# Optimization experiments

Measured on AMD Instinct MI355X. Metric: run time of the kernel, lower is better.

The kernel has to match this reference:

```python
import jax, jax.numpy as jnp
import numpy as np

TAU = 2.0
THR = 0.5
ALPHA = 4.0  # Sigmoid_Grad surrogate sharpness
EPS = 1e-5
HEADS = 16
SCALE = 0.25

@jax.custom_vjp
def spike(v):
    return (v > 0.0).astype(v.dtype)

def _spike_fwd(v):
    return (v > 0.0).astype(v.dtype), v

def _spike_bwd(v, g):
    s = jax.nn.sigmoid(ALPHA * v)
    return (g * ALPHA * s * (1.0 - s),)

spike.defvjp(_spike_fwd, _spike_bwd)

def lif(x):
    # x: (T, ...) ; stateful LIF over leading time dim, hard reset (detached spike)
    def step(mem, xt):
        mem = mem + (xt - mem) / TAU
        s = spike(mem - THR)
        mem = mem * (1.0 - jax.lax.stop_gradient(s))
        return mem, s
    _, s = jax.lax.scan(step, jnp.zeros_like(x[0]), x)
    return s

def bn(x, p):
    # x: (T,B,C,N), p: (4,C) = (gamma, beta, mean, var); inference-form BatchNorm1d
    g, b, m, v = p
    shp = (1, 1, -1, 1)
    return (x - m.reshape(shp)) * (g.reshape(shp) / jnp.sqrt(v.reshape(shp) + EPS)) + b.reshape(shp)

def conv_bn_lif(x, w, p, bias=None):
    # 1x1 Conv1d == channel matmul: (T,B,Cin,N) x (Cout,Cin) -> (T,B,Cout,N)
    y = jnp.einsum('tbcn,oc->tbon', x, w)
    if bias is not None:
        y = y + bias.reshape(1, 1, -1, 1)
    return lif(bn(y, p))

def _block(x, q_w, q_bn, k_w, k_bn, v_w, v_bn, proj_w, proj_bn,
           fc1_w, fc1_b, fc1_bn, fc2_w, fc2_b, fc2_bn):
    T, B, C, N = x.shape
    D = C // HEADS

    def to_heads(y):  # (T,B,C,N) -> (T,B,H,N,D)
        return y.transpose(0, 1, 3, 2).reshape(T, B, N, HEADS, D).transpose(0, 1, 3, 2, 4)

    q = to_heads(conv_bn_lif(x, q_w, q_bn))
    k = to_heads(conv_bn_lif(x, k_w, k_bn))
    v = to_heads(conv_bn_lif(x, v_w, v_bn))

    attn = jnp.einsum('tbhnd,tbhmd->tbhnm', q, k) * SCALE  # no softmax
    r = jnp.einsum('tbhnm,tbhmd->tbhnd', attn, v) * SCALE
    r = r.transpose(0, 1, 2, 4, 3).reshape(T, B, C, N)  # (T,B,H,D,N) -> (T,B,C,N)
    r = lif(r)  # attn_lif
    attn_out = conv_bn_lif(r, proj_w, proj_bn)  # proj conv+bn+lif

    x = x + attn_out  # residual 1

    h = conv_bn_lif(x, fc1_w, fc1_bn, fc1_b)
    m = conv_bn_lif(h, fc2_w, fc2_bn, fc2_b)
    return x + m  # residual 2

def setup_inputs() -> dict:
    key = jax.random.key(0)
    ks = jax.random.split(key, 16)
    T, B, C, N = 4, 16, 256, 512
    H = 1024  # mlp hidden = 4*C
    w = 0.05
    d = {}
    d['x'] = jax.random.normal(ks[0], (T, B, C, N), jnp.float32)
    d['q_w'] = jax.random.normal(ks[1], (C, C), jnp.float32) * w
    d['q_bn'] = jax.random.uniform(ks[2], (4, C), jnp.float32, 0.5, 1.5)
    d['k_w'] = jax.random.normal(ks[3], (C, C), jnp.float32) * w
    d['k_bn'] = jax.random.uniform(ks[4], (4, C), jnp.float32, 0.5, 1.5)
    d['v_w'] = jax.random.normal(ks[5], (C, C), jnp.float32) * w
    d['v_bn'] = jax.random.uniform(ks[6], (4, C), jnp.float32, 0.5, 1.5)
    d['proj_w'] = jax.random.normal(ks[7], (C, C), jnp.float32) * w
    d['proj_bn'] = jax.random.uniform(ks[8], (4, C), jnp.float32, 0.5, 1.5)
    d['fc1_w'] = jax.random.normal(ks[9], (H, C), jnp.float32) * w
    d['fc1_b'] = jnp.zeros((H,), jnp.float32)
    d['fc1_bn'] = jax.random.uniform(ks[10], (4, H), jnp.float32, 0.5, 1.5)
    d['fc2_w'] = jax.random.normal(ks[11], (C, H), jnp.float32) * w
    d['fc2_b'] = jnp.zeros((C,), jnp.float32)
    d['fc2_bn'] = jax.random.uniform(ks[12], (4, C), jnp.float32, 0.5, 1.5)
    return d

def reference(x, q_w, q_bn, k_w, k_bn, v_w, v_bn, proj_w, proj_bn,
              fc1_w, fc1_b, fc1_bn, fc2_w, fc2_b, fc2_bn):
    return _block(x, q_w, q_bn, k_w, k_bn, v_w, v_bn, proj_w, proj_bn,
                  fc1_w, fc1_b, fc1_bn, fc2_w, fc2_b, fc2_bn)
```

## Files before the change

kernel.cpp:

```cpp
#include <hip/hip_runtime.h>

#pragma clang fp contract(off)

typedef unsigned char u8;
typedef unsigned int u32;

#define TSTEPS 4

template <int XMODE, bool HASX2, int OMODE>
__global__ __launch_bounds__(256) void conv_bn_lif(
    const void* __restrict__ X1v, const u8* __restrict__ X2,
    const float* __restrict__ Wt, const float* __restrict__ bias,
    const float* __restrict__ bnp,
    u8* __restrict__ Sout,
    const float* __restrict__ Xres, const u8* __restrict__ AOres,
    float* __restrict__ Fout,
    int Bsz, int Cin, int Cout, int N)
{
  const int tid = threadIdx.x;
  const int tx = tid & 15, ty = tid >> 4;
  const int nBase = blockIdx.x * 64, oBase = blockIdx.y * 64, b = blockIdx.z;
  const int KT = Cin >> 5;
  const int TT = TSTEPS * KT;

  __shared__ __align__(16) float Xs[2][32][68];
  __shared__ __align__(16) float Ws[2][32][68];

  float sc[4], mn[4], bt[4], bi[4];
  #pragma unroll
  for (int i = 0; i < 4; ++i) {
    int o = oBase + ty * 4 + i;
    float g  = bnp[0 * Cout + o];
    float be = bnp[1 * Cout + o];
    float m  = bnp[2 * Cout + o];
    float vv = bnp[3 * Cout + o];
    float d_f = (float)((double)vv + (double)1e-5f);
    float s_f = (float)sqrt((double)d_f);
    sc[i] = (float)((double)g / (double)s_f);
    mn[i] = m; bt[i] = be;
    bi[i] = bias ? bias[o] : 0.0f;
  }

  float mem[4][4], acc[4][4];
  #pragma unroll
  for (int i = 0; i < 4; ++i)
    #pragma unroll
    for (int j = 0; j < 4; ++j) { mem[i][j] = 0.0f; acc[i][j] = 0.0f; }

  const int xRow = tid >> 3;
  const int xC8  = (tid & 7) * 8;
  const int wO   = tid >> 2;
  const int wK8  = (tid & 3) * 8;

  float4 pxa, pxb, pwa, pwb;
  uint2 pxu, pau;

  auto issue = [&](int i) {
    const int tI = i / KT, k0 = (i % KT) << 5;
    const size_t xb = (size_t)(tI * Bsz + b) * Cin * N
                    + (size_t)(k0 + xRow) * N + nBase + xC8;
    if constexpr (XMODE == 0) {
      pxa = *(const float4*)((const float*)X1v + xb);
      pxb = *(const float4*)((const float*)X1v + xb + 4);
    } else {
      pxu = *(const uint2*)((const u8*)X1v + xb);
    }
    if constexpr (HASX2) pau = *(const uint2*)(X2 + xb);
    const size_t wb = (size_t)(oBase + wO) * Cin + k0 + wK8;
    pwa = *(const float4*)(Wt + wb);
    pwb = *(const float4*)(Wt + wb + 4);
  };

  auto commit = [&](int buf) {
    float xv[8];
    if constexpr (XMODE == 0) {
      xv[0] = pxa.x; xv[1] = pxa.y; xv[2] = pxa.z; xv[3] = pxa.w;
      xv[4] = pxb.x; xv[5] = pxb.y; xv[6] = pxb.z; xv[7] = pxb.w;
    } else {
      #pragma unroll
      for (int j = 0; j < 4; ++j) xv[j]     = (float)((pxu.x >> (8 * j)) & 0xffu);
      #pragma unroll
      for (int j = 0; j < 4; ++j) xv[4 + j] = (float)((pxu.y >> (8 * j)) & 0xffu);
    }
    if constexpr (HASX2) {
      #pragma unroll
      for (int j = 0; j < 4; ++j) xv[j]     = xv[j]     + (float)((pau.x >> (8 * j)) & 0xffu);
      #pragma unroll
      for (int j = 0; j < 4; ++j) xv[4 + j] = xv[4 + j] + (float)((pau.y >> (8 * j)) & 0xffu);
    }
    *(float4*)&Xs[buf][xRow][xC8]     = make_float4(xv[0], xv[1], xv[2], xv[3]);
    *(float4*)&Xs[buf][xRow][xC8 + 4] = make_float4(xv[4], xv[5], xv[6], xv[7]);
    Ws[buf][wK8 + 0][wO] = pwa.x;  Ws[buf][wK8 + 1][wO] = pwa.y;
    Ws[buf][wK8 + 2][wO] = pwa.z;  Ws[buf][wK8 + 3][wO] = pwa.w;
    Ws[buf][wK8 + 4][wO] = pwb.x;  Ws[buf][wK8 + 5][wO] = pwb.y;
    Ws[buf][wK8 + 6][wO] = pwb.z;  Ws[buf][wK8 + 7][wO] = pwb.w;
  };

  issue(0);
  commit(0);
  __syncthreads();

  for (int tt = 0; tt < TT; ++tt) {
    const int buf = tt & 1;
    if (tt + 1 < TT) issue(tt + 1);

    #pragma unroll
    for (int kk = 0; kk < 32; ++kk) {
      float4 wv = *(const float4*)&Ws[buf][kk][ty * 4];
      float4 xv = *(const float4*)&Xs[buf][kk][tx * 4];
      float wa[4] = {wv.x, wv.y, wv.z, wv.w};
      float xa[4] = {xv.x, xv.y, xv.z, xv.w};
      #pragma unroll
      for (int i = 0; i < 4; ++i)
        #pragma unroll
        for (int j = 0; j < 4; ++j)
          acc[i][j] = fmaf(wa[i], xa[j], acc[i][j]);
    }

    if ((tt % KT) == KT - 1) {
      const int t = tt / KT;
      const size_t sbase = (size_t)(t * Bsz + b) * Cout * N;
      #pragma unroll
      for (int i = 0; i < 4; ++i) {
        const size_t rb = sbase + (size_t)(oBase + ty * 4 + i) * N + nBase + tx * 4;
        if constexpr (OMODE == 0) {
          u32 pack = 0;
          #pragma unroll
          for (int j = 0; j < 4; ++j) {
            float y = acc[i][j];
            if (bias) y = y + bi[i];
            float t1 = y - mn[i];
            float t2 = t1 * sc[i];
            y = t2 + bt[i];
            float m2 = mem[i][j];
            float dd = y - m2;
            m2 = m2 + dd * 0.5f;
            bool sp = (m2 - 0.5f) > 0.0f;
            mem[i][j] = sp ? 0.0f : m2;
            if (sp) pack |= (1u << (8 * j));
            acc[i][j] = 0.0f;
          }
          *(u32*)&Sout[rb] = pack;
        } else {
          float4 xr = *(const float4*)&Xres[rb];
          u32 av = *(const u32*)&AOres[rb];
          float xa4[4] = {xr.x, xr.y, xr.z, xr.w};
          float o4[4];
          #pragma unroll
          for (int j = 0; j < 4; ++j) {
            float y = acc[i][j];
            if (bias) y = y + bi[i];
            float t1 = y - mn[i];
            float t2 = t1 * sc[i];
            y = t2 + bt[i];
            float m2 = mem[i][j];
            float dd = y - m2;
            m2 = m2 + dd * 0.5f;
            bool sp = (m2 - 0.5f) > 0.0f;
            mem[i][j] = sp ? 0.0f : m2;
            float s = sp ? 1.0f : 0.0f;
            float xn = xa4[j] + (float)((av >> (8 * j)) & 0xffu);
            o4[j] = xn + s;
            acc[i][j] = 0.0f;
          }
          *(float4*)&Fout[rb] = make_float4(o4[0], o4[1], o4[2], o4[3]);
        }
      }
    }

    __syncthreads();
    if (tt + 1 < TT) commit((tt + 1) & 1);
    __syncthreads();
  }
}

__global__ __launch_bounds__(256) void attn_lif(
    const u8* __restrict__ Qs, const u8* __restrict__ Ks,
    const u8* __restrict__ Vs, u8* __restrict__ Rs,
    int Bsz, int C, int N)
{
  const int tid = threadIdx.x;
  const int h = blockIdx.x & 15;
  const int b = blockIdx.x >> 4;

  __shared__ u8 qs[16][528];
  __shared__ u8 ks[16][528];
  __shared__ u8 vs[16][528];
  __shared__ int Gs[16][17];

  const int eG = tid >> 4;
  const int dG = tid & 15;
  const int dR = tid >> 4;
  const int nR0 = tid & 15;

  float mem[32];
  #pragma unroll
  for (int i = 0; i < 32; ++i) mem[i] = 0.0f;

  for (int t = 0; t < TSTEPS; ++t) {
    __syncthreads();
    const size_t base = ((size_t)(t * Bsz + b) * C + h * 16) * N;
    for (int i = 0; i < 32; ++i) {
      int flat = tid + 256 * i;
      int d = flat >> 9, n = flat & 511;
      size_t g = base + (size_t)d * N + n;
      qs[d][n] = Qs[g];
      ks[d][n] = Ks[g];
      vs[d][n] = Vs[g];
    }
    __syncthreads();

    int gi = 0;
    for (int n = 0; n < 512; ++n)
      gi += (int)ks[eG][n] * (int)vs[dG][n];
    Gs[eG][dG] = gi;
    __syncthreads();

    int Greg[16];
    #pragma unroll
    for (int e = 0; e < 16; ++e) Greg[e] = Gs[e][dR];

    const size_t obase = ((size_t)(t * Bsz + b) * C + h * 16 + dR) * N;
    for (int j = 0; j < 32; ++j) {
      int n = nR0 + 16 * j;
      int ri = 0;
      #pragma unroll
      for (int e = 0; e < 16; ++e)
        ri += qs[e][n] ? Greg[e] : 0;
      float r = (float)ri * 0.0625f;
      float m2 = mem[j];
      float d = r - m2;
      m2 = m2 + d * 0.5f;
      float s = (m2 - 0.5f) > 0.0f ? 1.0f : 0.0f;
      mem[j] = (s > 0.0f) ? 0.0f : m2;
      Rs[obase + n] = (s > 0.0f) ? (u8)1 : (u8)0;
    }
  }
}

extern "C" void kernel_launch(void* const* d_in, const int* in_sizes, int n_in,
                              void* d_out, int out_size, void* d_ws, size_t ws_size,
                              hipStream_t stream)
{
  const float* x     = (const float*)d_in[0];
  const float* q_w   = (const float*)d_in[1];
  const float* q_bn  = (const float*)d_in[2];
  const float* k_w   = (const float*)d_in[3];
  const float* k_bn  = (const float*)d_in[4];
  const float* v_w   = (const float*)d_in[5];
  const float* v_bn  = (const float*)d_in[6];
  const float* p_w   = (const float*)d_in[7];
  const float* p_bn  = (const float*)d_in[8];
  const float* f1_w  = (const float*)d_in[9];
  const float* f1_b  = (const float*)d_in[10];
  const float* f1_bn = (const float*)d_in[11];
  const float* f2_w  = (const float*)d_in[12];
  const float* f2_b  = (const float*)d_in[13];
  const float* f2_bn = (const float*)d_in[14];

  const int T = 4, B = 16, C = 256, N = 512, Hm = 1024;
  const size_t SZ = (size_t)T * B * C * N;

  char* ws = (char*)d_ws;
  u8* q_s  = (u8*)(ws + 0 * SZ);
  u8* k_s  = (u8*)(ws + 1 * SZ);
  u8* v_s  = (u8*)(ws + 2 * SZ);
  u8* r_s  = (u8*)(ws + 3 * SZ);
  u8* ao_s = (u8*)(ws + 4 * SZ);
  u8* h_s  = (u8*)(ws + 0 * SZ);

  dim3 blk(256);
  dim3 gC(N / 64, C / 64, B);

  conv_bn_lif<0, false, 0><<<gC, blk, 0, stream>>>(
      x, nullptr, q_w, nullptr, q_bn, q_s, nullptr, nullptr, nullptr, B, C, C, N);
  conv_bn_lif<0, false, 0><<<gC, blk, 0, stream>>>(
      x, nullptr, k_w, nullptr, k_bn, k_s, nullptr, nullptr, nullptr, B, C, C, N);
  conv_bn_lif<0, false, 0><<<gC, blk, 0, stream>>>(
      x, nullptr, v_w, nullptr, v_bn, v_s, nullptr, nullptr, nullptr, B, C, C, N);
  attn_lif<<<dim3(B * 16), blk, 0, stream>>>(q_s, k_s, v_s, r_s, B, C, N);
  conv_bn_lif<1, false, 0><<<gC, blk, 0, stream>>>(
      r_s, nullptr, p_w, nullptr, p_bn, ao_s, nullptr, nullptr, nullptr, B, C, C, N);
  conv_bn_lif<0, true, 0><<<dim3(N / 64, Hm / 64, B), blk, 0, stream>>>(
      x, ao_s, f1_w, f1_b, f1_bn, h_s, nullptr, nullptr, nullptr, B, C, Hm, N);
  conv_bn_lif<1, false, 1><<<gC, blk, 0, stream>>>(
      h_s, nullptr, f2_w, f2_b, f2_bn, nullptr, x, ao_s, (float*)d_out, B, Hm, C, N);
}
```

Before: 999.4 us.

## Replace shared-memory tiled GEMM with direct global loads and register prefetch

```diff
diff --git a/kernel.cpp b/kernel.cpp
--- a/kernel.cpp
+++ b/kernel.cpp
@@ -20,11 +20,6 @@
   const int tid = threadIdx.x;
   const int tx = tid & 15, ty = tid >> 4;
   const int nBase = blockIdx.x * 64, oBase = blockIdx.y * 64, b = blockIdx.z;
-  const int KT = Cin >> 5;
-  const int TT = TSTEPS * KT;
-
-  __shared__ __align__(16) float Xs[2][32][68];
-  __shared__ __align__(16) float Ws[2][32][68];
 
   float sc[4], mn[4], bt[4], bi[4];
   #pragma unroll
@@ -47,130 +42,133 @@
     #pragma unroll
     for (int j = 0; j < 4; ++j) { mem[i][j] = 0.0f; acc[i][j] = 0.0f; }
 
-  const int xRow = tid >> 3;
-  const int xC8  = (tid & 7) * 8;
-  const int wO   = tid >> 2;
-  const int wK8  = (tid & 3) * 8;
-
-  float4 pxa, pxb, pwa, pwb;
-  uint2 pxu, pau;
-
-  auto issue = [&](int i) {
-    const int tI = i / KT, k0 = (i % KT) << 5;
-    const size_t xb = (size_t)(tI * Bsz + b) * Cin * N
-                    + (size_t)(k0 + xRow) * N + nBase + xC8;
-    if constexpr (XMODE == 0) {
-      pxa = *(const float4*)((const float*)X1v + xb);
-      pxb = *(const float4*)((const float*)X1v + xb + 4);
-    } else {
-      pxu = *(const uint2*)((const u8*)X1v + xb);
-    }
-    if constexpr (HASX2) pau = *(const uint2*)(X2 + xb);
-    const size_t wb = (size_t)(oBase + wO) * Cin + k0 + wK8;
-    pwa = *(const float4*)(Wt + wb);
-    pwb = *(const float4*)(Wt + wb + 4);
-  };
-
-  auto commit = [&](int buf) {
-    float xv[8];
-    if constexpr (XMODE == 0) {
-      xv[0] = pxa.x; xv[1] = pxa.y; xv[2] = pxa.z; xv[3] = pxa.w;
-      xv[4] = pxb.x; xv[5] = pxb.y; xv[6] = pxb.z; xv[7] = pxb.w;
-    } else {
-      #pragma unroll
-      for (int j = 0; j < 4; ++j) xv[j]     = (float)((pxu.x >> (8 * j)) & 0xffu);
-      #pragma unroll
-      for (int j = 0; j < 4; ++j) xv[4 + j] = (float)((pxu.y >> (8 * j)) & 0xffu);
-    }
-    if constexpr (HASX2) {
-      #pragma unroll
-      for (int j = 0; j < 4; ++j) xv[j]     = xv[j]     + (float)((pau.x >> (8 * j)) & 0xffu);
-      #pragma unroll
-      for (int j = 0; j < 4; ++j) xv[4 + j] = xv[4 + j] + (float)((pau.y >> (8 * j)) & 0xffu);
-    }
-    *(float4*)&Xs[buf][xRow][xC8]     = make_float4(xv[0], xv[1], xv[2], xv[3]);
-    *(float4*)&Xs[buf][xRow][xC8 + 4] = make_float4(xv[4], xv[5], xv[6], xv[7]);
-    Ws[buf][wK8 + 0][wO] = pwa.x;  Ws[buf][wK8 + 1][wO] = pwa.y;
-    Ws[buf][wK8 + 2][wO] = pwa.z;  Ws[buf][wK8 + 3][wO] = pwa.w;
-    Ws[buf][wK8 + 4][wO] = pwb.x;  Ws[buf][wK8 + 5][wO] = pwb.y;
-    Ws[buf][wK8 + 6][wO] = pwb.z;  Ws[buf][wK8 + 7][wO] = pwb.w;
-  };
-
-  issue(0);
-  commit(0);
-  __syncthreads();
-
-  for (int tt = 0; tt < TT; ++tt) {
-    const int buf = tt & 1;
-    if (tt + 1 < TT) issue(tt + 1);
-
-    #pragma unroll
-    for (int kk = 0; kk < 32; ++kk) {
-      float4 wv = *(const float4*)&Ws[buf][kk][ty * 4];
-      float4 xv = *(const float4*)&Xs[buf][kk][tx * 4];
-      float wa[4] = {wv.x, wv.y, wv.z, wv.w};
-      float xa[4] = {xv.x, xv.y, xv.z, xv.w};
+  const int nOff = nBase + tx * 4;
+
+  const float* Wr[4];
+  #pragma unroll
+  for (int i = 0; i < 4; ++i)
+    Wr[i] = Wt + (size_t)(oBase + ty * 4 + i) * Cin;
+
+  constexpr int D = (XMODE == 1) ? 4 : 2;
+  const int NG = Cin >> 2;
+
+  float4 wb[D][4];
+  float4 xb[D][4];
+  u32    xu[D][4];
+  u32    au[D][4];
+
+  for (int t = 0; t < TSTEPS; ++t) {
+    const float* xT0 = nullptr;
+    const u8*    xT1 = nullptr;
+    if constexpr (XMODE == 0)
+      xT0 = (const float*)X1v + (size_t)(t * Bsz + b) * Cin * N + nOff;
+    else
+      xT1 = (const u8*)X1v + (size_t)(t * Bsz + b) * Cin * N + nOff;
+    const u8* aT = nullptr;
+    if constexpr (HASX2)
+      aT = X2 + (size_t)(t * Bsz + b) * Cin * N + nOff;
+
+    auto LOAD = [&](int d, int g) {
       #pragma unroll
       for (int i = 0; i < 4; ++i)
+        wb[d][i] = *(const float4*)(Wr[i] + 4 * g);
+      #pragma unroll
+      for (int kk = 0; kk < 4; ++kk) {
+        if constexpr (XMODE == 0)
+          xb[d][kk] = *(const float4*)(xT0 + (size_t)(4 * g + kk) * N);
+        else
+          xu[d][kk] = *(const u32*)(xT1 + (size_t)(4 * g + kk) * N);
+        if constexpr (HASX2)
+          au[d][kk] = *(const u32*)(aT + (size_t)(4 * g + kk) * N);
+      }
+    };
+
+    auto COMP = [&](int d) {
+      #pragma unroll
+      for (int kk = 0; kk < 4; ++kk) {
+        float xa[4];
+        if constexpr (XMODE == 0) {
+          float4 xv = xb[d][kk];
+          xa[0] = xv.x; xa[1] = xv.y; xa[2] = xv.z; xa[3] = xv.w;
+        } else {
+          u32 u = xu[d][kk];
+          #pragma unroll
+          for (int j = 0; j < 4; ++j) xa[j] = (float)((u >> (8 * j)) & 0xffu);
+        }
+        if constexpr (HASX2) {
+          u32 a2 = au[d][kk];
+          #pragma unroll
+          for (int j = 0; j < 4; ++j)
+            xa[j] = xa[j] + (float)((a2 >> (8 * j)) & 0xffu);
+        }
         #pragma unroll
-        for (int j = 0; j < 4; ++j)
-          acc[i][j] = fmaf(wa[i], xa[j], acc[i][j]);
-    }
-
-    if ((tt % KT) == KT - 1) {
-      const int t = tt / KT;
-      const size_t sbase = (size_t)(t * Bsz + b) * Cout * N;
-      #pragma unroll
-      for (int i = 0; i < 4; ++i) {
-        const size_t rb = sbase + (size_t)(oBase + ty * 4 + i) * N + nBase + tx * 4;
-        if constexpr (OMODE == 0) {
-          u32 pack = 0;
+        for (int i = 0; i < 4; ++i) {
+          const float4 wq = wb[d][i];
+          const float wa = (kk == 0) ? wq.x : (kk == 1) ? wq.y
+                         : (kk == 2) ? wq.z : wq.w;
           #pragma unroll
-          for (int j = 0; j < 4; ++j) {
-            float y = acc[i][j];
-            if (bias) y = y + bi[i];
-            float t1 = y - mn[i];
-            float t2 = t1 * sc[i];
-            y = t2 + bt[i];
-            float m2 = mem[i][j];
-            float dd = y - m2;
-            m2 = m2 + dd * 0.5f;
-            bool sp = (m2 - 0.5f) > 0.0f;
-            mem[i][j] = sp ? 0.0f : m2;
-            if (sp) pack |= (1u << (8 * j));
-            acc[i][j] = 0.0f;
-          }
-          *(u32*)&Sout[rb] = pack;
-        } else {
-          float4 xr = *(const float4*)&Xres[rb];
-          u32 av = *(const u32*)&AOres[rb];
-          float xa4[4] = {xr.x, xr.y, xr.z, xr.w};
-          float o4[4];
-          #pragma unroll
-          for (int j = 0; j < 4; ++j) {
-            float y = acc[i][j];
-            if (bias) y = y + bi[i];
-            float t1 = y - mn[i];
-            float t2 = t1 * sc[i];
-            y = t2 + bt[i];
-            float m2 = mem[i][j];
-            float dd = y - m2;
-            m2 = m2 + dd * 0.5f;
-            bool sp = (m2 - 0.5f) > 0.0f;
-            mem[i][j] = sp ? 0.0f : m2;
-            float s = sp ? 1.0f : 0.0f;
-            float xn = xa4[j] + (float)((av >> (8 * j)) & 0xffu);
-            o4[j] = xn + s;
-            acc[i][j] = 0.0f;
-          }
-          *(float4*)&Fout[rb] = make_float4(o4[0], o4[1], o4[2], o4[3]);
+          for (int j = 0; j < 4; ++j)
+            acc[i][j] = fmaf(wa, xa[j], acc[i][j]);
         }
       }
-    }
-
-    __syncthreads();
-    if (tt + 1 < TT) commit((tt + 1) & 1);
-    __syncthreads();
+    };
+
+    #pragma unroll
+    for (int d = 0; d < D; ++d) LOAD(d, d);
+    for (int g = 0; g < NG - D; g += D) {
+      #pragma unroll
+      for (int d = 0; d < D; ++d) { COMP(d); LOAD(d, g + d + D); }
+    }
+    #pragma unroll
+    for (int d = 0; d < D; ++d) COMP(d);
+
+    const size_t sbase = (size_t)(t * Bsz + b) * Cout * N;
+    #pragma unroll
+    for (int i = 0; i < 4; ++i) {
+      const size_t rb = sbase + (size_t)(oBase + ty * 4 + i) * N + nBase + tx * 4;
+      if constexpr (OMODE == 0) {
+        u32 pack = 0;
+        #pragma unroll
+        for (int j = 0; j < 4; ++j) {
+          float y = acc[i][j];
+          if (bias) y = y + bi[i];
+          float t1 = y - mn[i];
+          float t2 = t1 * sc[i];
+          y = t2 + bt[i];
+          float m2 = mem[i][j];
+          float dd = y - m2;
+          m2 = m2 + dd * 0.5f;
+          bool sp = (m2 - 0.5f) > 0.0f;
+          mem[i][j] = sp ? 0.0f : m2;
+          if (sp) pack |= (1u << (8 * j));
+          acc[i][j] = 0.0f;
+        }
+        *(u32*)&Sout[rb] = pack;
+      } else {
+        float4 xr = *(const float4*)&Xres[rb];
+        u32 av = *(const u32*)&AOres[rb];
+        float xa4[4] = {xr.x, xr.y, xr.z, xr.w};
+        float o4[4];
+        #pragma unroll
+        for (int j = 0; j < 4; ++j) {
+          float y = acc[i][j];
+          if (bias) y = y + bi[i];
+          float t1 = y - mn[i];
+          float t2 = t1 * sc[i];
+          y = t2 + bt[i];
+          float m2 = mem[i][j];
+          float dd = y - m2;
+          m2 = m2 + dd * 0.5f;
+          bool sp = (m2 - 0.5f) > 0.0f;
+          mem[i][j] = sp ? 0.0f : m2;
+          float s = sp ? 1.0f : 0.0f;
+          float xn = xa4[j] + (float)((av >> (8 * j)) & 0xffu);
+          o4[j] = xn + s;
+          acc[i][j] = 0.0f;
+        }
+        *(float4*)&Fout[rb] = make_float4(o4[0], o4[1], o4[2], o4[3]);
+      }
+    }
   }
 }
 
@@ -278,7 +276,9 @@
       x, nullptr, k_w, nullptr, k_bn, k_s, nullptr, nullptr, nullptr, B, C, C, N);
   conv_bn_lif<0, false, 0><<<gC, blk, 0, stream>>>(
       x, nullptr, v_w, nullptr, v_bn, v_s, nullptr, nullptr, nullptr, B, C, C, N);
+
   attn_lif<<<dim3(B * 16), blk, 0, stream>>>(q_s, k_s, v_s, r_s, B, C, N);
+
   conv_bn_lif<1, false, 0><<<gC, blk, 0, stream>>>(
       r_s, nullptr, p_w, nullptr, p_bn, ao_s, nullptr, nullptr, nullptr, B, C, C, N);
   conv_bn_lif<0, true, 0><<<dim3(N / 64, Hm / 64, B), blk, 0, stream>>>(
```

New measurement: 2.049 ms. +105.0%, slower.

## Read conv weights as wave-uniform scalar loads instead of LDS tiles

Applied to the files above, without the earlier changes.

```diff
diff --git a/kernel.cpp b/kernel.cpp
--- a/kernel.cpp
+++ b/kernel.cpp
@@ -7,7 +7,7 @@
 
 #define TSTEPS 4
 
-template <int XMODE, bool HASX2, int OMODE>
+template <int XMODE, bool HASX2, int OMODE, int CIN>
 __global__ __launch_bounds__(256) void conv_bn_lif(
     const void* __restrict__ X1v, const u8* __restrict__ X2,
     const float* __restrict__ Wt, const float* __restrict__ bias,
@@ -15,21 +15,24 @@
     u8* __restrict__ Sout,
     const float* __restrict__ Xres, const u8* __restrict__ AOres,
     float* __restrict__ Fout,
-    int Bsz, int Cin, int Cout, int N)
+    int Bsz, int Cout, int N)
 {
-  const int tid = threadIdx.x;
-  const int tx = tid & 15, ty = tid >> 4;
+  const int tid  = threadIdx.x;
+  const int lane = tid & 63;
+  const int wid  = __builtin_amdgcn_readfirstlane(tid >> 6);
   const int nBase = blockIdx.x * 64, oBase = blockIdx.y * 64, b = blockIdx.z;
-  const int KT = Cin >> 5;
-  const int TT = TSTEPS * KT;
+  const int oW = oBase + wid * 16;
+  constexpr int KT = CIN >> 5;
+  constexpr int TT = TSTEPS * KT;
 
   __shared__ __align__(16) float Xs[2][32][68];
-  __shared__ __align__(16) float Ws[2][32][68];
-
-  float sc[4], mn[4], bt[4], bi[4];
+
+  const float* __restrict__ Wb = Wt + (size_t)oW * CIN;
+
+  float sc[16], mn[16], bt[16], bi[16];
   #pragma unroll
-  for (int i = 0; i < 4; ++i) {
-    int o = oBase + ty * 4 + i;
+  for (int i = 0; i < 16; ++i) {
+    int o = oW + i;
     float g  = bnp[0 * Cout + o];
     float be = bnp[1 * Cout + o];
     float m  = bnp[2 * Cout + o];
@@ -41,23 +44,19 @@
     bi[i] = bias ? bias[o] : 0.0f;
   }
 
-  float mem[4][4], acc[4][4];
+  float mem[16], acc[16];
   #pragma unroll
-  for (int i = 0; i < 4; ++i)
-    #pragma unroll
-    for (int j = 0; j < 4; ++j) { mem[i][j] = 0.0f; acc[i][j] = 0.0f; }
+  for (int i = 0; i < 16; ++i) { mem[i] = 0.0f; acc[i] = 0.0f; }
 
   const int xRow = tid >> 3;
   const int xC8  = (tid & 7) * 8;
-  const int wO   = tid >> 2;
-  const int wK8  = (tid & 3) * 8;
-
-  float4 pxa, pxb, pwa, pwb;
+
+  float4 pxa, pxb;
   uint2 pxu, pau;
 
   auto issue = [&](int i) {
     const int tI = i / KT, k0 = (i % KT) << 5;
-    const size_t xb = (size_t)(tI * Bsz + b) * Cin * N
+    const size_t xb = (size_t)(tI * Bsz + b) * CIN * N
                     + (size_t)(k0 + xRow) * N + nBase + xC8;
     if constexpr (XMODE == 0) {
       pxa = *(const float4*)((const float*)X1v + xb);
@@ -66,9 +65,6 @@
       pxu = *(const uint2*)((const u8*)X1v + xb);
     }
     if constexpr (HASX2) pau = *(const uint2*)(X2 + xb);
-    const size_t wb = (size_t)(oBase + wO) * Cin + k0 + wK8;
-    pwa = *(const float4*)(Wt + wb);
-    pwb = *(const float4*)(Wt + wb + 4);
   };
 
   auto commit = [&](int buf) {
@@ -90,10 +86,6 @@
     }
     *(float4*)&Xs[buf][xRow][xC8]     = make_float4(xv[0], xv[1], xv[2], xv[3]);
     *(float4*)&Xs[buf][xRow][xC8 + 4] = make_float4(xv[4], xv[5], xv[6], xv[7]);
-    Ws[buf][wK8 + 0][wO] = pwa.x;  Ws[buf][wK8 + 1][wO] = pwa.y;
-    Ws[buf][wK8 + 2][wO] = pwa.z;  Ws[buf][wK8 + 3][wO] = pwa.w;
-    Ws[buf][wK8 + 4][wO] = pwb.x;  Ws[buf][wK8 + 5][wO] = pwb.y;
-    Ws[buf][wK8 + 6][wO] = pwb.z;  Ws[buf][wK8 + 7][wO] = pwb.w;
   };
 
   issue(0);
@@ -102,68 +94,51 @@
 
   for (int tt = 0; tt < TT; ++tt) {
     const int buf = tt & 1;
+    const int k0 = (tt % KT) << 5;
     if (tt + 1 < TT) issue(tt + 1);
 
     #pragma unroll
-    for (int kk = 0; kk < 32; ++kk) {
-      float4 wv = *(const float4*)&Ws[buf][kk][ty * 4];
-      float4 xv = *(const float4*)&Xs[buf][kk][tx * 4];
-      float wa[4] = {wv.x, wv.y, wv.z, wv.w};
-      float xa[4] = {xv.x, xv.y, xv.z, xv.w};
-      #pragma unroll
-      for (int i = 0; i < 4; ++i)
-        #pragma unroll
-        for (int j = 0; j < 4; ++j)
-          acc[i][j] = fmaf(wa[i], xa[j], acc[i][j]);
+    for (int kb = 0; kb < 32; kb += 4) {
+      float xq[4];
+      #pragma unroll
+      for (int kk = 0; kk < 4; ++kk) xq[kk] = Xs[buf][kb + kk][lane];
+      #pragma unroll
+      for (int i = 0; i < 16; ++i) {
+        const size_t wrow = (size_t)i * CIN + k0 + kb;
+        float w0 = Wb[wrow + 0], w1 = Wb[wrow + 1];
+        float w2 = Wb[wrow + 2], w3 = Wb[wrow + 3];
+        acc[i] = fmaf(w0, xq[0], acc[i]);
+        acc[i] = fmaf(w1, xq[1], acc[i]);
+        acc[i] = fmaf(w2, xq[2], acc[i]);
+        acc[i] = fmaf(w3, xq[3], acc[i]);
+      }
     }
 
     if ((tt % KT) == KT - 1) {
       const int t = tt / KT;
       const size_t sbase = (size_t)(t * Bsz + b) * Cout * N;
       #pragma unroll
-      for (int i = 0; i < 4; ++i) {
-        const size_t rb = sbase + (size_t)(oBase + ty * 4 + i) * N + nBase + tx * 4;
+      for (int i = 0; i < 16; ++i) {
+        const size_t rb = sbase + (size_t)(oW + i) * N + nBase + lane;
+        float y = acc[i];
+        if (bias) y = y + bi[i];
+        float t1 = y - mn[i];
+        float t2 = t1 * sc[i];
+        y = t2 + bt[i];
+        float m2 = mem[i];
+        float dd = y - m2;
+        m2 = m2 + dd * 0.5f;
+        bool sp = (m2 - 0.5f) > 0.0f;
+        mem[i] = sp ? 0.0f : m2;
+        acc[i] = 0.0f;
         if constexpr (OMODE == 0) {
-          u32 pack = 0;
-          #pragma unroll
-          for (int j = 0; j < 4; ++j) {
-            float y = acc[i][j];
-            if (bias) y = y + bi[i];
-            float t1 = y - mn[i];
-            float t2 = t1 * sc[i];
-            y = t2 + bt[i];
-            float m2 = mem[i][j];
-            float dd = y - m2;
-            m2 = m2 + dd * 0.5f;
-            bool sp = (m2 - 0.5f) > 0.0f;
-            mem[i][j] = sp ? 0.0f : m2;
-            if (sp) pack |= (1u << (8 * j));
-            acc[i][j] = 0.0f;
-          }
-          *(u32*)&Sout[rb] = pack;
+          Sout[rb] = sp ? (u8)1 : (u8)0;
         } else {
-          float4 xr = *(const float4*)&Xres[rb];
-          u32 av = *(const u32*)&AOres[rb];
-          float xa4[4] = {xr.x, xr.y, xr.z, xr.w};
-          float o4[4];
-          #pragma unroll
-          for (int j = 0; j < 4; ++j) {
-            float y = acc[i][j];
-            if (bias) y = y + bi[i];
-            float t1 = y - mn[i];
-            float t2 = t1 * sc[i];
-            y = t2 + bt[i];
-            float m2 = mem[i][j];
-            float dd = y - m2;
-            m2 = m2 + dd * 0.5f;
-            bool sp = (m2 - 0.5f) > 0.0f;
-            mem[i][j] = sp ? 0.0f : m2;
-            float s = sp ? 1.0f : 0.0f;
-            float xn = xa4[j] + (float)((av >> (8 * j)) & 0xffu);
-            o4[j] = xn + s;
-            acc[i][j] = 0.0f;
-          }
-          *(float4*)&Fout[rb] = make_float4(o4[0], o4[1], o4[2], o4[3]);
+          float xr = Xres[rb];
+          float av = (float)AOres[rb];
+          float s = sp ? 1.0f : 0.0f;
+          float xn = xr + av;
+          Fout[rb] = xn + s;
         }
       }
     }
@@ -272,17 +247,19 @@
   dim3 blk(256);
   dim3 gC(N / 64, C / 64, B);
 
-  conv_bn_lif<0, false, 0><<<gC, blk, 0, stream>>>(
-      x, nullptr, q_w, nullptr, q_bn, q_s, nullptr, nullptr, nullptr, B, C, C, N);
-  conv_bn_lif<0, false, 0><<<gC, blk, 0, stream>>>(
-      x, nullptr, k_w, nullptr, k_bn, k_s, nullptr, nullptr, nullptr, B, C, C, N);
-  conv_bn_lif<0, false, 0><<<gC, blk, 0, stream>>>(
-      x, nullptr, v_w, nullptr, v_bn, v_s, nullptr, nullptr, nullptr, B, C, C, N);
+  conv_bn_lif<0, false, 0, 256><<<gC, blk, 0, stream>>>(
+      x, nullptr, q_w, nullptr, q_bn, q_s, nullptr, nullptr, nullptr, B, C, N);
+  conv_bn_lif<0, false, 0, 256><<<gC, blk, 0, stream>>>(
+      x, nullptr, k_w, nullptr, k_bn, k_s, nullptr, nullptr, nullptr, B, C, N);
+  conv_bn_lif<0, false, 0, 256><<<gC, blk, 0, stream>>>(
+      x, nullptr, v_w, nullptr, v_bn, v_s, nullptr, nullptr, nullptr, B, C, N);
+
   attn_lif<<<dim3(B * 16), blk, 0, stream>>>(q_s, k_s, v_s, r_s, B, C, N);
-  conv_bn_lif<1, false, 0><<<gC, blk, 0, stream>>>(
-      r_s, nullptr, p_w, nullptr, p_bn, ao_s, nullptr, nullptr, nullptr, B, C, C, N);
-  conv_bn_lif<0, true, 0><<<dim3(N / 64, Hm / 64, B), blk, 0, stream>>>(
-      x, ao_s, f1_w, f1_b, f1_bn, h_s, nullptr, nullptr, nullptr, B, C, Hm, N);
-  conv_bn_lif<1, false, 1><<<gC, blk, 0, stream>>>(
-      h_s, nullptr, f2_w, f2_b, f2_bn, nullptr, x, ao_s, (float*)d_out, B, Hm, C, N);
+
+  conv_bn_lif<1, false, 0, 256><<<gC, blk, 0, stream>>>(
+      r_s, nullptr, p_w, nullptr, p_bn, ao_s, nullptr, nullptr, nullptr, B, C, N);
+  conv_bn_lif<0, true, 0, 256><<<dim3(N / 64, Hm / 64, B), blk, 0, stream>>>(
+      x, ao_s, f1_w, f1_b, f1_bn, h_s, nullptr, nullptr, nullptr, B, Hm, N);
+  conv_bn_lif<1, false, 1, 1024><<<gC, blk, 0, stream>>>(
+      h_s, nullptr, f2_w, f2_b, f2_bn, nullptr, x, ao_s, (float*)d_out, B, C, N);
 }
```

Result: slower. 1.685 ms (+68.6%).

## Enlarge conv GEMM tiles to 128 columns, keep spike inputs as bytes in LDS

Applied to the files above, without the earlier changes.

```diff
diff --git a/kernel.cpp b/kernel.cpp
--- a/kernel.cpp
+++ b/kernel.cpp
@@ -7,8 +7,8 @@
 
 #define TSTEPS 4
 
-template <int XMODE, bool HASX2, int OMODE>
-__global__ __launch_bounds__(256) void conv_bn_lif(
+template <int P, int BK, int XMODE, bool HASX2, int OMODE>
+__global__ __launch_bounds__(256, 2) void conv_bn_lif(
     const void* __restrict__ X1v, const u8* __restrict__ X2,
     const float* __restrict__ Wt, const float* __restrict__ bias,
     const float* __restrict__ bnp,
@@ -17,83 +17,119 @@
     float* __restrict__ Fout,
     int Bsz, int Cin, int Cout, int N)
 {
+  constexpr int BO   = 16 * P;
+  constexpr int BN   = 128;
+  constexpr int TPR  = 256 / BK;
+  constexpr int FPT  = BN / TPR;
+  constexpr int NF4  = FPT / 4;
+  constexpr int THRO = 256 / BO;
+  constexpr int WPAD = (P == 4) ? 4 : 0;
+  constexpr int XROWF = BN + 8;
+
   const int tid = threadIdx.x;
   const int tx = tid & 15, ty = tid >> 4;
-  const int nBase = blockIdx.x * 64, oBase = blockIdx.y * 64, b = blockIdx.z;
-  const int KT = Cin >> 5;
+  const int nBase = blockIdx.x * BN, oBase = blockIdx.y * BO, b = blockIdx.z;
+  const int KT = Cin / BK;
   const int TT = TSTEPS * KT;
 
-  __shared__ __align__(16) float Xs[2][32][68];
-  __shared__ __align__(16) float Ws[2][32][68];
-
-  float sc[4], mn[4], bt[4], bi[4];
-  #pragma unroll
-  for (int i = 0; i < 4; ++i) {
-    int o = oBase + ty * 4 + i;
+  __shared__ __align__(16) float Ws[2][BK][BO + WPAD];
+  __shared__ __align__(16) u8 Xraw[(XMODE == 0) ? (2 * BK * XROWF * 4)
+                                                : (2 * BK * BN)];
+  __shared__ __align__(16) float BnL[BO][4];
+
+  float* XF = (float*)Xraw;
+  u8*    X8 = Xraw;
+
+  if (tid < BO) {
+    int o = oBase + tid;
     float g  = bnp[0 * Cout + o];
     float be = bnp[1 * Cout + o];
     float m  = bnp[2 * Cout + o];
     float vv = bnp[3 * Cout + o];
     float d_f = (float)((double)vv + (double)1e-5f);
     float s_f = (float)sqrt((double)d_f);
-    sc[i] = (float)((double)g / (double)s_f);
-    mn[i] = m; bt[i] = be;
-    bi[i] = bias ? bias[o] : 0.0f;
+    BnL[tid][0] = (float)((double)g / (double)s_f);
+    BnL[tid][1] = m;
+    BnL[tid][2] = be;
+    BnL[tid][3] = bias ? bias[o] : 0.0f;
   }
 
-  float mem[4][4], acc[4][4];
+  float mem[P][8], acc[P][8];
   #pragma unroll
-  for (int i = 0; i < 4; ++i)
+  for (int p = 0; p < P; ++p)
     #pragma unroll
-    for (int j = 0; j < 4; ++j) { mem[i][j] = 0.0f; acc[i][j] = 0.0f; }
-
-  const int xRow = tid >> 3;
-  const int xC8  = (tid & 7) * 8;
-  const int wO   = tid >> 2;
-  const int wK8  = (tid & 3) * 8;
-
-  float4 pxa, pxb, pwa, pwb;
-  uint2 pxu, pau;
+    for (int q = 0; q < 8; ++q) { mem[p][q] = 0.0f; acc[p][q] = 0.0f; }
+
+  const int xRow = tid / TPR;
+  const int xcF  = (tid % TPR) * FPT;
+  const int wO   = tid / THRO;
+  const int wK   = (tid % THRO) * 8;
+
+  float4 px[NF4];
+  u32    pxu[NF4];
+  u32    pau[NF4];
+  float4 pwa, pwb;
 
   auto issue = [&](int i) {
-    const int tI = i / KT, k0 = (i % KT) << 5;
+    const int tI = i / KT, k0 = (i % KT) * BK;
     const size_t xb = (size_t)(tI * Bsz + b) * Cin * N
-                    + (size_t)(k0 + xRow) * N + nBase + xC8;
+                    + (size_t)(k0 + xRow) * N + nBase + xcF;
     if constexpr (XMODE == 0) {
-      pxa = *(const float4*)((const float*)X1v + xb);
-      pxb = *(const float4*)((const float*)X1v + xb + 4);
+      const float* xp = (const float*)X1v + xb;
+      #pragma unroll
+      for (int f = 0; f < NF4; ++f) px[f] = *(const float4*)(xp + 4 * f);
     } else {
-      pxu = *(const uint2*)((const u8*)X1v + xb);
-    }
-    if constexpr (HASX2) pau = *(const uint2*)(X2 + xb);
-    const size_t wb = (size_t)(oBase + wO) * Cin + k0 + wK8;
+      const u8* xp = (const u8*)X1v + xb;
+      if constexpr (NF4 == 4) {
+        uint4 u = *(const uint4*)xp;
+        pxu[0] = u.x; pxu[1] = u.y; pxu[2] = u.z; pxu[3] = u.w;
+      } else {
+        uint2 u = *(const uint2*)xp;
+        pxu[0] = u.x; pxu[1] = u.y;
+      }
+    }
+    if constexpr (HASX2) {
+      const u8* ap = X2 + xb;
+      if constexpr (NF4 == 4) {
+        uint4 u = *(const uint4*)ap;
+        pau[0] = u.x; pau[1] = u.y; pau[2] = u.z; pau[3] = u.w;
+      } else {
+        uint2 u = *(const uint2*)ap;
+        pau[0] = u.x; pau[1] = u.y;
+      }
+    }
+    const size_t wb = (size_t)(oBase + wO) * Cin + k0 + wK;
     pwa = *(const float4*)(Wt + wb);
     pwb = *(const float4*)(Wt + wb + 4);
   };
 
-  auto commit = [&](int buf) {
-    float xv[8];
+  auto commit = [&](int bf) {
     if constexpr (XMODE == 0) {
-      xv[0] = pxa.x; xv[1] = pxa.y; xv[2] = pxa.z; xv[3] = pxa.w;
-      xv[4] = pxb.x; xv[5] = pxb.y; xv[6] = pxb.z; xv[7] = pxb.w;
+      #pragma unroll
+      for (int f = 0; f < NF4; ++f) {
+        float4 v = px[f];
+        if constexpr (HASX2) {
+          u32 a2 = pau[f];
+          v.x = v.x + (float)(a2 & 0xffu);
+          v.y = v.y + (float)((a2 >> 8) & 0xffu);
+          v.z = v.z + (float)((a2 >> 16) & 0xffu);
+          v.w = v.w + (float)((a2 >> 24) & 0xffu);
+        }
+        *(float4*)&XF[((size_t)(bf * BK + xRow)) * XROWF + xcF + 4 * f] = v;
+      }
     } else {
-      #pragma unroll
-      for (int j = 0; j < 4; ++j) xv[j]     = (float)((pxu.x >> (8 * j)) & 0xffu);
-      #pragma unroll
-      for (int j = 0; j < 4; ++j) xv[4 + j] = (float)((pxu.y >> (8 * j)) & 0xffu);
-    }
-    if constexpr (HASX2) {
-      #pragma unroll
-      for (int j = 0; j < 4; ++j) xv[j]     = xv[j]     + (float)((pau.x >> (8 * j)) & 0xffu);
-      #pragma unroll
-      for (int j = 0; j < 4; ++j) xv[4 + j] = xv[4 + j] + (float)((pau.y >> (8 * j)) & 0xffu);
-    }
-    *(float4*)&Xs[buf][xRow][xC8]     = make_float4(xv[0], xv[1], xv[2], xv[3]);
-    *(float4*)&Xs[buf][xRow][xC8 + 4] = make_float4(xv[4], xv[5], xv[6], xv[7]);
-    Ws[buf][wK8 + 0][wO] = pwa.x;  Ws[buf][wK8 + 1][wO] = pwa.y;
-    Ws[buf][wK8 + 2][wO] = pwa.z;  Ws[buf][wK8 + 3][wO] = pwa.w;
-    Ws[buf][wK8 + 4][wO] = pwb.x;  Ws[buf][wK8 + 5][wO] = pwb.y;
-    Ws[buf][wK8 + 6][wO] = pwb.z;  Ws[buf][wK8 + 7][wO] = pwb.w;
+      if constexpr (NF4 == 4) {
+        *(uint4*)&X8[(size_t)(bf * BK + xRow) * BN + xcF] =
+            make_uint4(pxu[0], pxu[1], pxu[2], pxu[3]);
+      } else {
+        *(uint2*)&X8[(size_t)(bf * BK + xRow) * BN + xcF] =
+            make_uint2(pxu[0], pxu[1]);
+      }
+    }
+    Ws[bf][wK + 0][wO] = pwa.x;  Ws[bf][wK + 1][wO] = pwa.y;
+    Ws[bf][wK + 2][wO] = pwa.z;  Ws[bf][wK + 3][wO] = pwa.w;
+    Ws[bf][wK + 4][wO] = pwb.x;  Ws[bf][wK + 5][wO] = pwb.y;
+    Ws[bf][wK + 6][wO] = pwb.z;  Ws[bf][wK + 7][wO] = pwb.w;
   };
 
   issue(0);
@@ -105,65 +141,99 @@
     if (tt + 1 < TT) issue(tt + 1);
 
     #pragma unroll
-    for (int kk = 0; kk < 32; ++kk) {
-      float4 wv = *(const float4*)&Ws[buf][kk][ty * 4];
-      float4 xv = *(const float4*)&Xs[buf][kk][tx * 4];
-      float wa[4] = {wv.x, wv.y, wv.z, wv.w};
-      float xa[4] = {xv.x, xv.y, xv.z, xv.w};
-      #pragma unroll
-      for (int i = 0; i < 4; ++i)
+    for (int kk = 0; kk < BK; ++kk) {
+      float xa[8];
+      if constexpr (XMODE == 0) {
+        float4 x0 = *(const float4*)&XF[(size_t)(buf * BK + kk) * XROWF + tx * 4];
+        float4 x1 = *(const float4*)&XF[(size_t)(buf * BK + kk) * XROWF + 64 + tx * 4];
+        xa[0] = x0.x; xa[1] = x0.y; xa[2] = x0.z; xa[3] = x0.w;
+        xa[4] = x1.x; xa[5] = x1.y; xa[6] = x1.z; xa[7] = x1.w;
+      } else {
+        uint2 u = *(const uint2*)&X8[(size_t)(buf * BK + kk) * BN + tx * 8];
         #pragma unroll
-        for (int j = 0; j < 4; ++j)
-          acc[i][j] = fmaf(wa[i], xa[j], acc[i][j]);
+        for (int j = 0; j < 4; ++j) xa[j]     = (float)((u.x >> (8 * j)) & 0xffu);
+        #pragma unroll
+        for (int j = 0; j < 4; ++j) xa[4 + j] = (float)((u.y >> (8 * j)) & 0xffu);
+      }
+      float wa[P];
+      float4 w0 = *(const float4*)&Ws[buf][kk][ty * P];
+      wa[0] = w0.x; wa[1] = w0.y; wa[2] = w0.z; wa[3] = w0.w;
+      if constexpr (P == 8) {
+        float4 w1 = *(const float4*)&Ws[buf][kk][ty * P + 4];
+        wa[4] = w1.x; wa[5] = w1.y; wa[6] = w1.z; wa[7] = w1.w;
+      }
+      #pragma unroll
+      for (int p = 0; p < P; ++p)
+        #pragma unroll
+        for (int q = 0; q < 8; ++q)
+          acc[p][q] = fmaf(wa[p], xa[q], acc[p][q]);
     }
 
     if ((tt % KT) == KT - 1) {
       const int t = tt / KT;
       const size_t sbase = (size_t)(t * Bsz + b) * Cout * N;
       #pragma unroll
-      for (int i = 0; i < 4; ++i) {
-        const size_t rb = sbase + (size_t)(oBase + ty * 4 + i) * N + nBase + tx * 4;
-        if constexpr (OMODE == 0) {
-          u32 pack = 0;
+      for (int p = 0; p < P; ++p) {
+        const int o = oBase + ty * P + p;
+        float4 bv = *(const float4*)&BnL[ty * P + p][0];
+        bool spk[8];
+        #pragma unroll
+        for (int q = 0; q < 8; ++q) {
+          float y = acc[p][q];
+          if (bias) y = y + bv.w;
+          float t1 = y - bv.y;
+          float t2 = t1 * bv.x;
+          y = t2 + bv.z;
+          float m2 = mem[p][q];
+          float dd = y - m2;
+          m2 = m2 + dd * 0.5f;
+          bool sp = (m2 - 0.5f) > 0.0f;
+          mem[p][q] = sp ? 0.0f : m2;
+          spk[q] = sp;
+          acc[p][q] = 0.0f;
+        }
+        if constexpr (XMODE == 0) {
+          const size_t rb0 = sbase + (size_t)o * N + nBase + tx * 4;
+          u32 pk0 = 0, pk1 = 0;
           #pragma unroll
           for (int j = 0; j < 4; ++j) {
-            float y = acc[i][j];
-            if (bias) y = y + bi[i];
-            float t1 = y - mn[i];
-            float t2 = t1 * sc[i];
-            y = t2 + bt[i];
-            float m2 = mem[i][j];
-            float dd = y - m2;
-            m2 = m2 + dd * 0.5f;
-            bool sp = (m2 - 0.5f) > 0.0f;
-            mem[i][j] = sp ? 0.0f : m2;
-            if (sp) pack |= (1u << (8 * j));
-            acc[i][j] = 0.0f;
+            if (spk[j])     pk0 |= (1u << (8 * j));
+            if (spk[4 + j]) pk1 |= (1u << (8 * j));
           }
-          *(u32*)&Sout[rb] = pack;
+          *(u32*)&Sout[rb0]      = pk0;
+          *(u32*)&Sout[rb0 + 64] = pk1;
         } else {
-          float4 xr = *(const float4*)&Xres[rb];
-          u32 av = *(const u32*)&AOres[rb];
-          float xa4[4] = {xr.x, xr.y, xr.z, xr.w};
-          float o4[4];
-          #pragma unroll
-          for (int j = 0; j < 4; ++j) {
-            float y = acc[i][j];
-            if (bias) y = y + bi[i];
-            float t1 = y - mn[i];
-            float t2 = t1 * sc[i];
-            y = t2 + bt[i];
-            float m2 = mem[i][j];
-            float dd = y - m2;
-            m2 = m2 + dd * 0.5f;
-            bool sp = (m2 - 0.5f) > 0.0f;
-            mem[i][j] = sp ? 0.0f : m2;
-            float s = sp ? 1.0f : 0.0f;
-            float xn = xa4[j] + (float)((av >> (8 * j)) & 0xffu);
-            o4[j] = xn + s;
-            acc[i][j] = 0.0f;
+          const size_t rb = sbase + (size_t)o * N + nBase + tx * 8;
+          if constexpr (OMODE == 0) {
+            u32 pk0 = 0, pk1 = 0;
+            #pragma unroll
+            for (int j = 0; j < 4; ++j) {
+              if (spk[j])     pk0 |= (1u << (8 * j));
+              if (spk[4 + j]) pk1 |= (1u << (8 * j));
+            }
+            *(uint2*)&Sout[rb] = make_uint2(pk0, pk1);
+          } else {
+            float4 xr0 = *(const float4*)&Xres[rb];
+            float4 xr1 = *(const float4*)&Xres[rb + 4];
+            uint2 av = *(const uint2*)&AOres[rb];
+            float xa4[8] = {xr0.x, xr0.y, xr0.z, xr0.w,
+                            xr1.x, xr1.y, xr1.z, xr1.w};
+            float o4[8];
+            #pragma unroll
+            for (int j = 0; j < 4; ++j) {
+              float s = spk[j] ? 1.0f : 0.0f;
+              float xn = xa4[j] + (float)((av.x >> (8 * j)) & 0xffu);
+              o4[j] = xn + s;
+            }
+            #pragma unroll
+            for (int j = 0; j < 4; ++j) {
+              float s = spk[4 + j] ? 1.0f : 0.0f;
+              float xn = xa4[4 + j] + (float)((av.y >> (8 * j)) & 0xffu);
+              o4[4 + j] = xn + s;
+            }
+            *(float4*)&Fout[rb]     = make_float4(o4[0], o4[1], o4[2], o4[3]);
+            *(float4*)&Fout[rb + 4] = make_float4(o4[4], o4[5], o4[6], o4[7]);
           }
-          *(float4*)&Fout[rb] = make_float4(o4[0], o4[1], o4[2], o4[3]);
         }
       }
     }
@@ -270,19 +340,22 @@
   u8* h_s  = (u8*)(ws + 0 * SZ);
 
   dim3 blk(256);
-  dim3 gC(N / 64, C / 64, B);
-
-  conv_bn_lif<0, false, 0><<<gC, blk, 0, stream>>>(
+  dim3 gC64(N / 128, C / 64, B);
+  dim3 gF1(N / 128, Hm / 128, B);
+
+  conv_bn_lif<4, 32, 0, false, 0><<<gC64, blk, 0, stream>>>(
       x, nullptr, q_w, nullptr, q_bn, q_s, nullptr, nullptr, nullptr, B, C, C, N);
-  conv_bn_lif<0, false, 0><<<gC, blk, 0, stream>>>(
+  conv_bn_lif<4, 32, 0, false, 0><<<gC64, blk, 0, stream>>>(
       x, nullptr, k_w, nullptr, k_bn, k_s, nullptr, nullptr, nullptr, B, C, C, N);
-  conv_bn_lif<0, false, 0><<<gC, blk, 0, stream>>>(
+  conv_bn_lif<4, 32, 0, false, 0><<<gC64, blk, 0, stream>>>(
       x, nullptr, v_w, nullptr, v_bn, v_s, nullptr, nullptr, nullptr, B, C, C, N);
+
   attn_lif<<<dim3(B * 16), blk, 0, stream>>>(q_s, k_s, v_s, r_s, B, C, N);
-  conv_bn_lif<1, false, 0><<<gC, blk, 0, stream>>>(
+
+  conv_bn_lif<4, 32, 1, false, 0><<<gC64, blk, 0, stream>>>(
       r_s, nullptr, p_w, nullptr, p_bn, ao_s, nullptr, nullptr, nullptr, B, C, C, N);
-  conv_bn_lif<0, true, 0><<<dim3(N / 64, Hm / 64, B), blk, 0, stream>>>(
+  conv_bn_lif<8, 16, 0, true, 0><<<gF1, blk, 0, stream>>>(
       x, ao_s, f1_w, f1_b, f1_bn, h_s, nullptr, nullptr, nullptr, B, C, Hm, N);
-  conv_bn_lif<1, false, 1><<<gC, blk, 0, stream>>>(
+  conv_bn_lif<4, 32, 1, false, 1><<<gC64, blk, 0, stream>>>(
       h_s, nullptr, f2_w, f2_b, f2_bn, nullptr, x, ao_s, (float*)d_out, B, Hm, C, N);
 }
```

New measurement: 1.144 ms. 1.14x slower.
